# Optimization experiments

Measured on AMD Instinct MI355X. Metric: run time of the kernel, lower is better.

## Reference

```python
import jax, jax.numpy as jnp
import numpy as np

TIMESTEPS = 8
NUM_HEADS = 16
CTX = 1024
D = 1024
HD = D // NUM_HEADS
LN_EPS = 1e-5


def setup_inputs() -> dict:
    key = jax.random.key(0)
    ks = jax.random.split(key, 16)
    s = 0.02
    return {
        "current_embs": jax.random.normal(ks[0], (4, CTX, D), jnp.float32),
        "emb_table": jax.random.normal(ks[1], (TIMESTEPS, D), jnp.float32) * s,
        "Wq": jax.random.normal(ks[2], (NUM_HEADS, D, HD), jnp.float32) * s,
        "Wk": jax.random.normal(ks[3], (NUM_HEADS, D, HD), jnp.float32) * s,
        "Wv": jax.random.normal(ks[4], (NUM_HEADS, D, HD), jnp.float32) * s,
        "fc_w": jax.random.normal(ks[5], (D, D), jnp.float32) * s,
        "fc_b": jnp.zeros((D,), jnp.float32),
        "ln1_w": jnp.ones((D,), jnp.float32),
        "ln1_b": jnp.zeros((D,), jnp.float32),
        "ln2_w": jnp.ones((D,), jnp.float32),
        "ln2_b": jnp.zeros((D,), jnp.float32),
        "mlp_w1": jax.random.normal(ks[6], (D, 2 * D), jnp.float32) * s,
        "mlp_b1": jnp.zeros((2 * D,), jnp.float32),
        "mlp_w2": jax.random.normal(ks[7], (2 * D, D), jnp.float32) * s,
        "mlp_b2": jnp.zeros((D,), jnp.float32),
        "mlp_w3": jax.random.normal(ks[8], (D, D), jnp.float32) * s,
        "mlp_b3": jnp.zeros((D,), jnp.float32),
    }


def _layernorm(x, w, b):
    mu = jnp.mean(x, axis=-1, keepdims=True)
    var = jnp.var(x, axis=-1, keepdims=True)
    return (x - mu) * jax.lax.rsqrt(var + LN_EPS) * w + b


def _block(x, Wq, Wk, Wv, fc_w, fc_b, ln1_w, ln1_b, ln2_w, ln2_b,
           mlp_w1, mlp_b1, mlp_w2, mlp_b2, mlp_w3, mlp_b3):
    B, T, C = x.shape
    h = _layernorm(x, ln1_w, ln1_b)
    # per-head projections: [B,H,T,HD]
    q = jnp.einsum("btd,hdk->bhtk", h, Wq)
    k = jnp.einsum("btd,hdk->bhtk", h, Wk)
    v = jnp.einsum("btd,hdk->bhtk", h, Wv)
    # NOTE: original scales by embed_size**-0.5 (C), not head_dim**-0.5
    wei = jnp.einsum("bhtk,bhsk->bhts", q, k) * (C ** -0.5)
    causal = jnp.tril(jnp.ones((T, T), bool))
    wei = jnp.where(causal, wei, -jnp.inf)
    wei = jax.nn.softmax(wei, axis=-1)
    attn = jnp.einsum("bhts,bhsk->bhtk", wei, v)  # [B,H,T,HD]
    attn = attn.transpose(0, 2, 1, 3).reshape(B, T, C)  # concat heads
    sa = attn @ fc_w + fc_b
    x = x + sa  # dropout is identity in eval mode
    h2 = _layernorm(x, ln2_w, ln2_b)
    m = ((h2 @ mlp_w1 + mlp_b1) @ mlp_w2 + mlp_b2) @ mlp_w3 + mlp_b3
    m = jax.nn.gelu(m, approximate=False)  # GELU after three stacked Linears, as in source
    return x + m


def reference(current_embs, emb_table, Wq, Wk, Wv, fc_w, fc_b,
              ln1_w, ln1_b, ln2_w, ln2_b,
              mlp_w1, mlp_b1, mlp_w2, mlp_b2, mlp_w3, mlp_b3):
    new_embs = current_embs
    for i in range(TIMESTEPS):
        current_embs = current_embs + new_embs + emb_table[i][None, None, :]
        new_embs = _block(current_embs, Wq, Wk, Wv, fc_w, fc_b,
                          ln1_w, ln1_b, ln2_w, ln2_b,
                          mlp_w1, mlp_b1, mlp_w2, mlp_b2, mlp_w3, mlp_b3)
    return new_embs
```

## Files before the change

kernel.cpp:

```cpp
#include <hip/hip_runtime.h>
#include <hip/hip_bf16.h>
#include <math.h>

typedef __bf16 bf16;
typedef __bf16 bf16x8 __attribute__((ext_vector_type(8)));
typedef __bf16 bf16x4 __attribute__((ext_vector_type(4)));
typedef short  s16x4  __attribute__((ext_vector_type(4)));
typedef float  f32x4  __attribute__((ext_vector_type(4)));

#define MFMA32(a,b,c) __builtin_amdgcn_mfma_f32_16x16x32_bf16((a),(b),(c),0,0,0)
#define MFMA16(a,b,c) __builtin_amdgcn_mfma_f32_16x16x16bf16_1k((a),(b),(c),0,0,0)
#define EXP2F(x) __builtin_amdgcn_exp2f(x)
#define GLL16(gp, lp) __builtin_amdgcn_global_load_lds(\
    (const __attribute__((address_space(1))) void*)(gp), \
    (__attribute__((address_space(3))) void*)(lp), 16, 0, 0)

__device__ __forceinline__ float wave_sum(float v){
#pragma unroll
  for(int off=1; off<64; off<<=1) v += __shfl_xor(v, off);
  return v;
}

__global__ __launch_bounds__(256) void add_ln_kernel(
    const float* __restrict__ xsrc, const float* __restrict__ addsrc,
    const float* __restrict__ emb,
    const float* __restrict__ gw, const float* __restrict__ gb,
    float* __restrict__ xout, bf16* __restrict__ hout)
{
  const int row = blockIdx.x;
  const int t = threadIdx.x;
  const size_t rbase = (size_t)row * 1024;
  float4 x = ((const float4*)(xsrc + rbase))[t];
  if(addsrc){
    float4 a = ((const float4*)(addsrc + rbase))[t];
    x.x += a.x; x.y += a.y; x.z += a.z; x.w += a.w;
  }
  if(emb){
    float4 e = ((const float4*)emb)[t];
    x.x += e.x; x.y += e.y; x.z += e.z; x.w += e.w;
  }
  if(xout) ((float4*)(xout + rbase))[t] = x;

  float s = x.x + x.y + x.z + x.w;
  float q = x.x*x.x + x.y*x.y + x.z*x.z + x.w*x.w;
  s = wave_sum(s); q = wave_sum(q);
  __shared__ float red[8];
  const int w = t >> 6;
  if((t & 63) == 0){ red[w] = s; red[4+w] = q; }
  __syncthreads();
  s = red[0]+red[1]+red[2]+red[3];
  q = red[4]+red[5]+red[6]+red[7];
  const float mean = s * (1.0f/1024.0f);
  const float var  = q * (1.0f/1024.0f) - mean*mean;
  const float inv  = rsqrtf(var + 1e-5f);

  float4 wv = ((const float4*)gw)[t];
  float4 bv = ((const float4*)gb)[t];
  bf16x4 hv;
  hv[0] = (bf16)((x.x - mean)*inv*wv.x + bv.x);
  hv[1] = (bf16)((x.y - mean)*inv*wv.y + bv.y);
  hv[2] = (bf16)((x.z - mean)*inv*wv.z + bv.z);
  hv[3] = (bf16)((x.w - mean)*inv*wv.w + bv.w);
  *(bf16x4*)(hout + rbase + t*4) = hv;
}

__global__ __launch_bounds__(256) void pack_qkv3_kernel(
    const float* __restrict__ Wq, const float* __restrict__ Wk, const float* __restrict__ Wv,
    bf16* __restrict__ Wt)
{
  const int i = blockIdx.x*256 + threadIdx.x;
  const int seg = i >> 20, j = i & 1048575;
  const float* W = (seg==0) ? Wq : (seg==1 ? Wk : Wv);
  const int n = j >> 10, d = j & 1023;
  const int h = n >> 6, kk = n & 63;
  Wt[i] = (bf16)W[h*65536 + d*64 + kk];
}
__global__ __launch_bounds__(256) void pack_t_kernel(const float* __restrict__ W, bf16* __restrict__ Wt, int Kd, int Nd){
  const int i = blockIdx.x*256 + threadIdx.x;
  const int n = i / Kd, k = i - n*Kd;
  Wt[i] = (bf16)W[(size_t)k*Nd + n];
}
__global__ __launch_bounds__(256) void pack_cast_kernel(const float* __restrict__ W, bf16* __restrict__ Wb){
  const int i = blockIdx.x*256 + threadIdx.x;
  Wb[i] = (bf16)W[i];
}
__global__ __launch_bounds__(256) void biasmv_kernel(const float* __restrict__ bin, const bf16* __restrict__ WT,
                                                     const float* __restrict__ badd, float* __restrict__ out, int Kd){
  const int n = blockIdx.x, t = threadIdx.x;
  float acc = 0.f;
  for(int k=t; k<Kd; k+=256) acc += bin[k]*(float)WT[(size_t)n*Kd + k];
  acc = wave_sum(acc);
  __shared__ float red[4];
  if((t&63)==0) red[t>>6] = acc;
  __syncthreads();
  if(t==0) out[n] = red[0]+red[1]+red[2]+red[3] + badd[n];
}

template<int EPI, int BLKM>
__global__ __launch_bounds__(256,2) void gemm_kernel(
    const bf16* __restrict__ A, const bf16* __restrict__ Bt,
    float* __restrict__ outf, bf16* __restrict__ outb,
    bf16* __restrict__ o2, bf16* __restrict__ o3,
    const float* __restrict__ bias, const float* __restrict__ res,
    const float* __restrict__ res2, const float* __restrict__ embn,
    int N, int K)
{
  constexpr int RM = BLKM/32;
  constexpr int HM = BLKM/2;
  constexpr int AISS = BLKM/32;
  __shared__ __align__(16) bf16 As[BLKM*64];
  __shared__ __align__(16) bf16 Bs[128*64];
  const int tid = threadIdx.x, w = tid>>6, lane = tid&63;
  const int quad = lane>>4, l16 = lane&15;
  const int wm = w&1, wn = w>>1;
  const int tn = blockIdx.x, tm = blockIdx.y;

  const int srow = lane>>3;
  const int sch  = (lane&7) ^ srow;
  const bf16* Ag = A  + (size_t)(tm*BLKM + w*8 + srow)*K + sch*8;
  const bf16* Bg = Bt + (size_t)(tn*128  + w*8 + srow)*K + sch*8;

  f32x4 acc[RM][4] = {};

  for(int k0 = 0; k0 < K; k0 += 64){
#pragma unroll
    for(int i=0;i<AISS;i++) GLL16(Ag + (size_t)(i*32)*K, As + (w*8 + i*32)*64);
#pragma unroll
    for(int i=0;i<4;i++)    GLL16(Bg + (size_t)(i*32)*K, Bs + (w*8 + i*32)*64);
    Ag += 64; Bg += 64;
    __syncthreads();
    bf16x8 af[RM][2], bfr[4][2];
#pragma unroll
    for(int r=0;r<RM;r++){
      const int row = wm*HM + r*16 + l16;
      const bf16* rp = As + row*64;
#pragma unroll
      for(int kc=0;kc<2;kc++)
        af[r][kc] = *(const bf16x8*)(rp + ((kc*4+quad) ^ (row&7))*8);
    }
#pragma unroll
    for(int c=0;c<4;c++){
      const int row = wn*64 + c*16 + l16;
      const bf16* rp = Bs + row*64;
#pragma unroll
      for(int kc=0;kc<2;kc++)
        bfr[c][kc] = *(const bf16x8*)(rp + ((kc*4+quad) ^ (row&7))*8);
    }
#pragma unroll
    for(int kc=0;kc<2;kc++)
#pragma unroll
      for(int r=0;r<RM;r++)
#pragma unroll
        for(int c=0;c<4;c++)
          acc[r][c] = MFMA32(af[r][kc], bfr[c][kc], acc[r][c]);
    __syncthreads();
  }

#pragma unroll
  for(int r=0;r<RM;r++){
    const int grow0 = tm*BLKM + wm*HM + r*16 + quad*4;
#pragma unroll
    for(int c=0;c<4;c++){
      const int gcol = tn*128 + wn*64 + c*16 + l16;
      float bv = 0.0f;
      if constexpr (EPI>=1 && EPI!=4) bv = bias[gcol];
      if constexpr (EPI==4){
        const int seg = gcol >> 10;
        if(seg < 2){
          bf16* op = (seg==0) ? outb : o2;
          const float qs = (seg==0) ? 0.045084439f : 1.0f;
          const int col = gcol & 1023;
#pragma unroll
          for(int g=0; g<4; g++)
            op[(size_t)(grow0+g)*1024 + col] = (bf16)(acc[r][c][g]*qs);
        } else {
          const int col0 = gcol & 1023, hh = col0>>6, kk = col0&63;
          const int btok = grow0>>10, t0 = grow0&1023;
          bf16x4 pv;
#pragma unroll
          for(int g=0; g<4; g++) pv[g] = (bf16)acc[r][c][g];
          *(bf16x4*)(o3 + ((size_t)(btok*16+hh)*64 + kk)*1024 + t0) = pv;
        }
      } else {
        const float ev = (EPI==5) ? embn[gcol] : 0.0f;
#pragma unroll
        for(int g=0; g<4; g++){
          const float vv = acc[r][c][g] + bv;
          const size_t idx = (size_t)(grow0+g)*N + gcol;
          if constexpr (EPI<=1){
            outb[idx] = (bf16)vv;
          } else if constexpr (EPI==2){
            outf[idx] = res[idx] + vv;
          } else if constexpr (EPI==3){
            const float gel = 0.5f*vv*(1.0f + erff(vv*0.70710678118654752f));
            outf[idx] = res[idx] + gel;
          } else {
            const float gel = 0.5f*vv*(1.0f + erff(vv*0.70710678118654752f));
            outf[idx] = res[idx] + gel + res2[idx] + ev;
          }
        }
      }
    }
  }
}

constexpr int KSZ = 64*64;

__global__ __launch_bounds__(256,4) void attn_kernel(
    const bf16* __restrict__ Q, const bf16* __restrict__ Km,
    const bf16* __restrict__ Vt, bf16* __restrict__ O)
{
  __shared__ __align__(16) bf16 Ks[2*KSZ];
  __shared__ __align__(16) bf16 Vs[2*KSZ];
  const int qt = blockIdx.y;
  const int bh = blockIdx.x;
  const int b = bh >> 4, h = bh & 15;
  const int tid = threadIdx.x;
  const int w = tid>>6, lane = tid&63, quad = lane>>4, l16 = lane&15;
  const size_t qbase = (size_t)b*1024*1024 + (size_t)h*64;
  const size_t vbase = (size_t)(bh*64)*1024;
  const int qrow0 = qt*64 + w*16;
  const int myrow = qrow0 + l16;

  const bf16* qp = Q + qbase + (size_t)myrow*1024 + quad*8;
  bf16x8 bq0 = *(const bf16x8*)qp, bq1 = *(const bf16x8*)(qp + 32);

  f32x4 o[4] = {};
  float l = 0.f;
  const f32x4 zf = {0.f,0.f,0.f,0.f};

  const int srow = lane>>3;
  const int sch  = (lane&7) ^ srow;
  const bf16* kg = Km + qbase + (size_t)(w*8 + srow)*1024 + sch*8;
  const bf16* vg = Vt + vbase + (size_t)(w*8 + srow)*1024 + sch*8;

  GLL16(kg,                       Ks + w*512);
  GLL16(kg + (size_t)32*1024,     Ks + 2048 + w*512);
  GLL16(vg,                       Vs + w*512);
  GLL16(vg + (size_t)32*1024,     Vs + 2048 + w*512);

  for(int kb = 0; kb <= qt; kb++){
    const int cur = kb & 1;
    __syncthreads();

    if(kb < qt){
      const bf16* kgp = kg + (size_t)(kb+1)*64*1024;
      const bf16* vgp = vg + (size_t)(kb+1)*64;
      bf16* kd = Ks + (cur^1)*KSZ + w*512;
      bf16* vd = Vs + (cur^1)*KSZ + w*512;
      GLL16(kgp,                   kd);
      GLL16(kgp + (size_t)32*1024, kd + 2048);
      GLL16(vgp,                   vd);
      GLL16(vgp + (size_t)32*1024, vd + 2048);
    }

    const bool diag = (kb == qt);
    const int nc = diag ? (w+1) : 4;
    const bf16* ksb = Ks + cur*KSZ;
    const bf16* vsb = Vs + cur*KSZ;

    f32x4 s[4];
#pragma unroll
    for(int c=0;c<4;c++){
      if(c >= nc) continue;
      const int row = c*16 + l16;
      const bf16* rp = ksb + row*64;
      bf16x8 ak0 = *(const bf16x8*)(rp + (( quad      ^ (row&7))<<3));
      bf16x8 ak1 = *(const bf16x8*)(rp + (((quad^4)   ^ (row&7))<<3));
      s[c] = MFMA32(ak0, bq0, zf);
      s[c] = MFMA32(ak1, bq1, s[c]);
    }

    s16x4 pp[4];
#pragma unroll
    for(int c=0;c<4;c++){
      if(c >= nc) continue;
      bf16x4 pb;
#pragma unroll
      for(int g=0;g<4;g++){
        const int key = kb*64 + c*16 + quad*4 + g;
        const float e = (diag && key > myrow) ? 0.f : EXP2F(s[c][g]);
        l += e; pb[g] = (bf16)e;
      }
      pp[c] = __builtin_bit_cast(s16x4, pb);
    }

#pragma unroll
    for(int c=0;c<4;c++){
      if(c >= nc) continue;
#pragma unroll
      for(int d=0;d<4;d++){
        const int row = d*16 + l16;
        const int eo  = ((((c*2 + (quad>>1)) ^ (row&7))<<3) + ((quad&1)<<2));
        bf16x4 av = *(const bf16x4*)(vsb + row*64 + eo);
        o[d] = MFMA16(__builtin_bit_cast(s16x4, av), pp[c], o[d]);
      }
    }
  }

  l += __shfl_xor(l, 16); l += __shfl_xor(l, 32);

  __syncthreads();
  {
    bf16* ot = Ks + w*(16*72);
    const float inv = 1.0f / l;
#pragma unroll
    for(int d=0;d<4;d++)
#pragma unroll
      for(int g=0;g<4;g++)
        ot[l16*72 + d*16 + quad*4 + g] = (bf16)(o[d][g]*inv);
#pragma unroll
    for(int p2=0;p2<2;p2++){
      const int qr = (lane>>3) + 8*p2, hd0 = (lane&7)*8;
      bf16x8 val = *(const bf16x8*)(ot + qr*72 + hd0);
      *(bf16x8*)(O + qbase + (size_t)(qrow0+qr)*1024 + hd0) = val;
    }
  }
}

extern "C" void kernel_launch(void* const* d_in, const int* in_sizes, int n_in,
                              void* d_out, int out_size, void* d_ws, size_t ws_size,
                              hipStream_t stream)
{
  const float* x_in = (const float*)d_in[0];
  const float* emb  = (const float*)d_in[1];
  const float* Wq   = (const float*)d_in[2];
  const float* Wk   = (const float*)d_in[3];
  const float* Wv   = (const float*)d_in[4];
  const float* fcw  = (const float*)d_in[5];
  const float* fcb  = (const float*)d_in[6];
  const float* ln1w = (const float*)d_in[7];
  const float* ln1b = (const float*)d_in[8];
  const float* ln2w = (const float*)d_in[9];
  const float* ln2b = (const float*)d_in[10];
  const float* w1   = (const float*)d_in[11];
  const float* b1   = (const float*)d_in[12];
  const float* w2   = (const float*)d_in[13];
  const float* b2   = (const float*)d_in[14];
  const float* w3   = (const float*)d_in[15];
  const float* b3   = (const float*)d_in[16];

  char* ws = (char*)d_ws;
  const size_t MB = 1024*1024;
  float* cur    = (float*)(ws + 0);
  float* x1     = (float*)(ws + 16*MB);
  bf16*  hb     = (bf16*)(ws + 48*MB);
  bf16*  attnb  = (bf16*)(ws + 56*MB);
  bf16*  qb     = (bf16*)(ws + 64*MB);
  bf16*  kbuf   = (bf16*)(ws + 72*MB);
  bf16*  vtb    = (bf16*)(ws + 80*MB);
  bf16*  w1pl   = (bf16*)(ws + 88*MB);
  bf16*  T12    = (bf16*)(ws + 92*MB);
  bf16*  wqkvT  = (bf16*)(ws + 96*MB);
  bf16*  fcT    = (bf16*)(ws + 102*MB);
  bf16*  w2T    = (bf16*)(ws + 104*MB);
  bf16*  w3T    = (bf16*)(ws + 108*MB);
  bf16*  WeffT  = (bf16*)(ws + 110*MB);
  float* tmpb   = (float*)(ws + 112*MB);
  float* beff   = (float*)(ws + 112*MB + 8192);

  pack_qkv3_kernel<<<12288,256,0,stream>>>(Wq, Wk, Wv, wqkvT);
  pack_t_kernel<<<4096,256,0,stream>>>(fcw, fcT, 1024, 1024);
  pack_t_kernel<<<8192,256,0,stream>>>(w2,  w2T, 2048, 1024);
  pack_t_kernel<<<4096,256,0,stream>>>(w3,  w3T, 1024, 1024);
  pack_cast_kernel<<<8192,256,0,stream>>>(w1, w1pl);
  gemm_kernel<0,64><<<dim3(8,16),256,0,stream>>>(w1pl, w2T, nullptr, T12,   nullptr, nullptr, nullptr, nullptr, nullptr, nullptr, 1024, 2048);
  gemm_kernel<0,64><<<dim3(8,16),256,0,stream>>>(w3T,  T12, nullptr, WeffT, nullptr, nullptr, nullptr, nullptr, nullptr, nullptr, 1024, 1024);
  biasmv_kernel<<<1024,256,0,stream>>>(b1,   w2T, b2, tmpb, 2048);
  biasmv_kernel<<<1024,256,0,stream>>>(tmpb, w3T, b3, beff, 1024);

  add_ln_kernel<<<4096,256,0,stream>>>(x_in, x_in, emb, ln1w, ln1b, cur, hb);
  for(int t=0; t<8; t++){
    if(t > 0)
      add_ln_kernel<<<4096,256,0,stream>>>(cur, nullptr, nullptr, ln1w, ln1b, nullptr, hb);
    gemm_kernel<4,128><<<dim3(24,32),256,0,stream>>>(hb, wqkvT, nullptr, qb, kbuf, vtb, nullptr, nullptr, nullptr, nullptr, 3072, 1024);
    attn_kernel<<<dim3(64,16),256,0,stream>>>(qb, kbuf, vtb, attnb);
    gemm_kernel<2,64><<<dim3(8,64),256,0,stream>>>(attnb, fcT, x1, nullptr, nullptr, nullptr, fcb, cur, nullptr, nullptr, 1024, 1024);
    add_ln_kernel<<<4096,256,0,stream>>>(x1, nullptr, nullptr, ln2w, ln2b, nullptr, hb);
    if(t < 7)
      gemm_kernel<5,64><<<dim3(8,64),256,0,stream>>>(hb, WeffT, cur, nullptr, nullptr, nullptr, beff, x1, cur, emb + (t+1)*1024, 1024, 1024);
    else
      gemm_kernel<3,64><<<dim3(8,64),256,0,stream>>>(hb, WeffT, (float*)d_out, nullptr, nullptr, nullptr, beff, x1, nullptr, nullptr, 1024, 1024);
  }
}
```

Baseline: 1.130 ms.

## Load attention K/V tiles directly from global memory instead of LDS staging

The attention kernel no longer double-buffers K and V tiles into shared memory with async global-to-LDS loads and block barriers. Each wave now reads its MFMA operands straight from global memory, relying on L1/L2 caching, and the per-block barriers are gone. The output staging uses a small dedicated buffer with vectorized bf16x4 stores, and the occupancy hint in the launch bounds is dropped. This removes synchronization and LDS traffic but adds redundant, less coalesced global loads across the four waves and exposes global latency without a prefetch.

After: 1.736 ms. +53.6%, slower.

```diff
diff --git a/kernel.cpp b/kernel.cpp
--- a/kernel.cpp
+++ b/kernel.cpp
@@ -204,14 +204,11 @@
   }
 }
 
-constexpr int KSZ = 64*64;
-
-__global__ __launch_bounds__(256,4) void attn_kernel(
+__global__ __launch_bounds__(256) void attn_kernel(
     const bf16* __restrict__ Q, const bf16* __restrict__ Km,
     const bf16* __restrict__ Vt, bf16* __restrict__ O)
 {
-  __shared__ __align__(16) bf16 Ks[2*KSZ];
-  __shared__ __align__(16) bf16 Vs[2*KSZ];
+  __shared__ __align__(16) bf16 obuf[4][16*72];
   const int qt = blockIdx.y;
   const int bh = blockIdx.x;
   const int b = bh >> 4, h = bh & 15;
@@ -225,48 +222,26 @@
   const bf16* qp = Q + qbase + (size_t)myrow*1024 + quad*8;
   bf16x8 bq0 = *(const bf16x8*)qp, bq1 = *(const bf16x8*)(qp + 32);
 
+  const bf16* kp = Km + qbase + (size_t)l16*1024 + quad*8;
+  const bf16* vp = Vt + vbase + (size_t)l16*1024 + quad*4;
+
   f32x4 o[4] = {};
   float l = 0.f;
   const f32x4 zf = {0.f,0.f,0.f,0.f};
 
-  const int srow = lane>>3;
-  const int sch  = (lane&7) ^ srow;
-  const bf16* kg = Km + qbase + (size_t)(w*8 + srow)*1024 + sch*8;
-  const bf16* vg = Vt + vbase + (size_t)(w*8 + srow)*1024 + sch*8;
-
-  GLL16(kg,                       Ks + w*512);
-  GLL16(kg + (size_t)32*1024,     Ks + 2048 + w*512);
-  GLL16(vg,                       Vs + w*512);
-  GLL16(vg + (size_t)32*1024,     Vs + 2048 + w*512);
-
   for(int kb = 0; kb <= qt; kb++){
-    const int cur = kb & 1;
-    __syncthreads();
-
-    if(kb < qt){
-      const bf16* kgp = kg + (size_t)(kb+1)*64*1024;
-      const bf16* vgp = vg + (size_t)(kb+1)*64;
-      bf16* kd = Ks + (cur^1)*KSZ + w*512;
-      bf16* vd = Vs + (cur^1)*KSZ + w*512;
-      GLL16(kgp,                   kd);
-      GLL16(kgp + (size_t)32*1024, kd + 2048);
-      GLL16(vgp,                   vd);
-      GLL16(vgp + (size_t)32*1024, vd + 2048);
-    }
-
     const bool diag = (kb == qt);
     const int nc = diag ? (w+1) : 4;
-    const bf16* ksb = Ks + cur*KSZ;
-    const bf16* vsb = Vs + cur*KSZ;
+    const bf16* kpb = kp + (size_t)kb*64*1024;
+    const bf16* vpb = vp + kb*64;
 
     f32x4 s[4];
 #pragma unroll
     for(int c=0;c<4;c++){
       if(c >= nc) continue;
-      const int row = c*16 + l16;
-      const bf16* rp = ksb + row*64;
-      bf16x8 ak0 = *(const bf16x8*)(rp + (( quad      ^ (row&7))<<3));
-      bf16x8 ak1 = *(const bf16x8*)(rp + (((quad^4)   ^ (row&7))<<3));
+      const bf16* rp = kpb + (size_t)(c*16)*1024;
+      bf16x8 ak0 = *(const bf16x8*)rp;
+      bf16x8 ak1 = *(const bf16x8*)(rp + 32);
       s[c] = MFMA32(ak0, bq0, zf);
       s[c] = MFMA32(ak1, bq1, s[c]);
     }
@@ -290,9 +265,7 @@
       if(c >= nc) continue;
 #pragma unroll
       for(int d=0;d<4;d++){
-        const int row = d*16 + l16;
-        const int eo  = ((((c*2 + (quad>>1)) ^ (row&7))<<3) + ((quad&1)<<2));
-        bf16x4 av = *(const bf16x4*)(vsb + row*64 + eo);
+        bf16x4 av = *(const bf16x4*)(vpb + (size_t)(d*16)*1024 + c*16);
         o[d] = MFMA16(__builtin_bit_cast(s16x4, av), pp[c], o[d]);
       }
     }
@@ -300,15 +273,16 @@
 
   l += __shfl_xor(l, 16); l += __shfl_xor(l, 32);
 
-  __syncthreads();
   {
-    bf16* ot = Ks + w*(16*72);
+    bf16* ot = obuf[w];
     const float inv = 1.0f / l;
 #pragma unroll
-    for(int d=0;d<4;d++)
-#pragma unroll
-      for(int g=0;g<4;g++)
-        ot[l16*72 + d*16 + quad*4 + g] = (bf16)(o[d][g]*inv);
+    for(int d=0;d<4;d++){
+      bf16x4 ob;
+#pragma unroll
+      for(int g=0;g<4;g++) ob[g] = (bf16)(o[d][g]*inv);
+      *(bf16x4*)(ot + l16*72 + d*16 + quad*4) = ob;
+    }
 #pragma unroll
     for(int p2=0;p2<2;p2++){
       const int qr = (lane>>3) + 8*p2, hd0 = (lane&7)*8;
```

## Fuse layernorm into GEMM prologue with row stats from producer epilogues

Applied to the files above, without the earlier changes.

Removes the per-step layernorm kernels. Producing GEMM epilogues now accumulate per-row sum and sum-of-squares with atomics into a stats buffer, and a new gemm_ln_kernel normalizes fp32 activations on the fly while staging the A tile to LDS. This drops the bf16 intermediate buffer writes and reads and two launches per timestep. In exchange, the A tile is re-read in fp32 by every column block, global atomics are added, and the A load loses async pipelining. The variance is computed as E[x^2]-mean^2.

New measurement: 1.443 ms. 27.7% more time.

```diff
diff --git a/kernel.cpp b/kernel.cpp
--- a/kernel.cpp
+++ b/kernel.cpp
@@ -21,25 +21,18 @@
   return v;
 }
 
-__global__ __launch_bounds__(256) void add_ln_kernel(
-    const float* __restrict__ xsrc, const float* __restrict__ addsrc,
-    const float* __restrict__ emb,
-    const float* __restrict__ gw, const float* __restrict__ gb,
-    float* __restrict__ xout, bf16* __restrict__ hout)
+__global__ __launch_bounds__(256) void add_stats_kernel(
+    const float* __restrict__ xsrc, const float* __restrict__ emb,
+    float* __restrict__ xout, float* __restrict__ ostats)
 {
   const int row = blockIdx.x;
   const int t = threadIdx.x;
   const size_t rbase = (size_t)row * 1024;
   float4 x = ((const float4*)(xsrc + rbase))[t];
-  if(addsrc){
-    float4 a = ((const float4*)(addsrc + rbase))[t];
-    x.x += a.x; x.y += a.y; x.z += a.z; x.w += a.w;
-  }
-  if(emb){
-    float4 e = ((const float4*)emb)[t];
-    x.x += e.x; x.y += e.y; x.z += e.z; x.w += e.w;
-  }
-  if(xout) ((float4*)(xout + rbase))[t] = x;
+  float4 e = ((const float4*)emb)[t];
+  x.x = 2.0f*x.x + e.x; x.y = 2.0f*x.y + e.y;
+  x.z = 2.0f*x.z + e.z; x.w = 2.0f*x.w + e.w;
+  ((float4*)(xout + rbase))[t] = x;
 
   float s = x.x + x.y + x.z + x.w;
   float q = x.x*x.x + x.y*x.y + x.z*x.z + x.w*x.w;
@@ -48,20 +41,14 @@
   const int w = t >> 6;
   if((t & 63) == 0){ red[w] = s; red[4+w] = q; }
   __syncthreads();
-  s = red[0]+red[1]+red[2]+red[3];
-  q = red[4]+red[5]+red[6]+red[7];
-  const float mean = s * (1.0f/1024.0f);
-  const float var  = q * (1.0f/1024.0f) - mean*mean;
-  const float inv  = rsqrtf(var + 1e-5f);
-
-  float4 wv = ((const float4*)gw)[t];
-  float4 bv = ((const float4*)gb)[t];
-  bf16x4 hv;
-  hv[0] = (bf16)((x.x - mean)*inv*wv.x + bv.x);
-  hv[1] = (bf16)((x.y - mean)*inv*wv.y + bv.y);
-  hv[2] = (bf16)((x.z - mean)*inv*wv.z + bv.z);
-  hv[3] = (bf16)((x.w - mean)*inv*wv.w + bv.w);
-  *(bf16x4*)(hout + rbase + t*4) = hv;
+  if(t == 0){
+    ostats[row]        = red[0]+red[1]+red[2]+red[3];
+    ostats[4096 + row] = red[4]+red[5]+red[6]+red[7];
+  }
+}
+
+__global__ __launch_bounds__(256) void zero_kernel(float* __restrict__ p){
+  ((float4*)p)[blockIdx.x*256 + threadIdx.x] = float4{0.f,0.f,0.f,0.f};
 }
 
 __global__ __launch_bounds__(256) void pack_qkv3_kernel(
@@ -100,10 +87,8 @@
 __global__ __launch_bounds__(256,2) void gemm_kernel(
     const bf16* __restrict__ A, const bf16* __restrict__ Bt,
     float* __restrict__ outf, bf16* __restrict__ outb,
-    bf16* __restrict__ o2, bf16* __restrict__ o3,
     const float* __restrict__ bias, const float* __restrict__ res,
-    const float* __restrict__ res2, const float* __restrict__ embn,
-    int N, int K)
+    float* __restrict__ ostats, int N, int K)
 {
   constexpr int RM = BLKM/32;
   constexpr int HM = BLKM/2;
@@ -156,6 +141,7 @@
     __syncthreads();
   }
 
+  float rs[RM][4] = {}, rq[RM][4] = {};
 #pragma unroll
   for(int r=0;r<RM;r++){
     const int grow0 = tm*BLKM + wm*HM + r*16 + quad*4;
@@ -163,7 +149,150 @@
     for(int c=0;c<4;c++){
       const int gcol = tn*128 + wn*64 + c*16 + l16;
       float bv = 0.0f;
-      if constexpr (EPI>=1 && EPI!=4) bv = bias[gcol];
+      if constexpr (EPI>=1) bv = bias[gcol];
+#pragma unroll
+      for(int g=0; g<4; g++){
+        const float vv = acc[r][c][g] + bv;
+        const size_t idx = (size_t)(grow0+g)*N + gcol;
+        if constexpr (EPI<=1){
+          outb[idx] = (bf16)vv;
+        } else {
+          const float ov = res[idx] + vv;
+          outf[idx] = ov;
+          rs[r][g] += ov; rq[r][g] += ov*ov;
+        }
+      }
+    }
+  }
+  if constexpr (EPI==2){
+#pragma unroll
+    for(int r=0;r<RM;r++)
+#pragma unroll
+      for(int g=0;g<4;g++){
+        float s1 = rs[r][g], s2 = rq[r][g];
+        s1 += __shfl_xor(s1,1); s2 += __shfl_xor(s2,1);
+        s1 += __shfl_xor(s1,2); s2 += __shfl_xor(s2,2);
+        s1 += __shfl_xor(s1,4); s2 += __shfl_xor(s2,4);
+        s1 += __shfl_xor(s1,8); s2 += __shfl_xor(s2,8);
+        if(l16 == 0){
+          const int row = tm*BLKM + wm*HM + r*16 + quad*4 + g;
+          atomicAdd(ostats + row, s1);
+          atomicAdd(ostats + 4096 + row, s2);
+        }
+      }
+  }
+}
+
+template<int EPI, int BLKM>
+__global__ __launch_bounds__(256,2) void gemm_ln_kernel(
+    const float* __restrict__ X, const float* __restrict__ stats,
+    const float* __restrict__ gw, const float* __restrict__ gb,
+    const bf16* __restrict__ Bt,
+    float* __restrict__ outf, bf16* __restrict__ outb,
+    bf16* __restrict__ o2, bf16* __restrict__ o3,
+    const float* __restrict__ bias, const float* __restrict__ res,
+    const float* __restrict__ res2, const float* __restrict__ embn,
+    float* __restrict__ ostats, int N)
+{
+  constexpr int RM  = BLKM/32;
+  constexpr int HM  = BLKM/2;
+  constexpr int RPT = BLKM/32;
+  __shared__ __align__(16) bf16 As[BLKM*64];
+  __shared__ __align__(16) bf16 Bs[128*64];
+  const int tid = threadIdx.x, w = tid>>6, lane = tid&63;
+  const int quad = lane>>4, l16 = lane&15;
+  const int wm = w&1, wn = w>>1;
+  const int tn = blockIdx.x, tm = blockIdx.y;
+
+  const int srow = lane>>3;
+  const int sch  = (lane&7) ^ srow;
+  const bf16* Bg = Bt + (size_t)(tn*128 + w*8 + srow)*1024 + sch*8;
+
+  const int c8  = tid & 7;
+  const int rr0 = (tid>>3)*RPT;
+  float mean_[RPT], inv_[RPT];
+#pragma unroll
+  for(int i=0;i<RPT;i++){
+    const int row = tm*BLKM + rr0 + i;
+    const float mu = stats[row]*(1.0f/1024.0f);
+    mean_[i] = mu;
+    inv_[i]  = rsqrtf(stats[4096+row]*(1.0f/1024.0f) - mu*mu + 1e-5f);
+  }
+  const float* xp = X + (size_t)(tm*BLKM + rr0)*1024 + c8*8;
+
+  float4 xa[RPT][2];
+#pragma unroll
+  for(int i=0;i<RPT;i++){
+    xa[i][0] = *(const float4*)(xp + (size_t)i*1024);
+    xa[i][1] = *(const float4*)(xp + (size_t)i*1024 + 4);
+  }
+  float4 gv0 = *(const float4*)(gw + c8*8), gv1 = *(const float4*)(gw + c8*8 + 4);
+  float4 bv0 = *(const float4*)(gb + c8*8), bv1 = *(const float4*)(gb + c8*8 + 4);
+
+  f32x4 acc[RM][4] = {};
+
+  for(int k0 = 0; k0 < 1024; k0 += 64){
+    __syncthreads();
+#pragma unroll
+    for(int i=0;i<RPT;i++){
+      bf16x8 hv;
+      hv[0] = (bf16)((xa[i][0].x - mean_[i])*inv_[i]*gv0.x + bv0.x);
+      hv[1] = (bf16)((xa[i][0].y - mean_[i])*inv_[i]*gv0.y + bv0.y);
+      hv[2] = (bf16)((xa[i][0].z - mean_[i])*inv_[i]*gv0.z + bv0.z);
+      hv[3] = (bf16)((xa[i][0].w - mean_[i])*inv_[i]*gv0.w + bv0.w);
+      hv[4] = (bf16)((xa[i][1].x - mean_[i])*inv_[i]*gv1.x + bv1.x);
+      hv[5] = (bf16)((xa[i][1].y - mean_[i])*inv_[i]*gv1.y + bv1.y);
+      hv[6] = (bf16)((xa[i][1].z - mean_[i])*inv_[i]*gv1.z + bv1.z);
+      hv[7] = (bf16)((xa[i][1].w - mean_[i])*inv_[i]*gv1.w + bv1.w);
+      *(bf16x8*)(As + (rr0+i)*64 + ((c8 ^ ((rr0+i)&7))<<3)) = hv;
+    }
+#pragma unroll
+    for(int i=0;i<4;i++) GLL16(Bg + (size_t)(i*32)*1024, Bs + (w*8 + i*32)*64);
+    Bg += 64;
+    __syncthreads();
+    if(k0 + 64 < 1024){
+      const float* xn = xp + k0 + 64;
+#pragma unroll
+      for(int i=0;i<RPT;i++){
+        xa[i][0] = *(const float4*)(xn + (size_t)i*1024);
+        xa[i][1] = *(const float4*)(xn + (size_t)i*1024 + 4);
+      }
+      gv0 = *(const float4*)(gw + k0+64 + c8*8); gv1 = *(const float4*)(gw + k0+64 + c8*8 + 4);
+      bv0 = *(const float4*)(gb + k0+64 + c8*8); bv1 = *(const float4*)(gb + k0+64 + c8*8 + 4);
+    }
+    bf16x8 af[RM][2], bfr[4][2];
+#pragma unroll
+    for(int r=0;r<RM;r++){
+      const int row = wm*HM + r*16 + l16;
+      const bf16* rp = As + row*64;
+#pragma unroll
+      for(int kc=0;kc<2;kc++)
+        af[r][kc] = *(const bf16x8*)(rp + ((kc*4+quad) ^ (row&7))*8);
+    }
+#pragma unroll
+    for(int c=0;c<4;c++){
+      const int row = wn*64 + c*16 + l16;
+      const bf16* rp = Bs + row*64;
+#pragma unroll
+      for(int kc=0;kc<2;kc++)
+        bfr[c][kc] = *(const bf16x8*)(rp + ((kc*4+quad) ^ (row&7))*8);
+    }
+#pragma unroll
+    for(int kc=0;kc<2;kc++)
+#pragma unroll
+      for(int r=0;r<RM;r++)
+#pragma unroll
+        for(int c=0;c<4;c++)
+          acc[r][c] = MFMA32(af[r][kc], bfr[c][kc], acc[r][c]);
+  }
+
+  float rs[RM][4] = {}, rq[RM][4] = {};
+#pragma unroll
+  for(int r=0;r<RM;r++){
+    const int grow0 = tm*BLKM + wm*HM + r*16 + quad*4;
+#pragma unroll
+    for(int c=0;c<4;c++){
+      const int gcol = tn*128 + wn*64 + c*16 + l16;
       if constexpr (EPI==4){
         const int seg = gcol >> 10;
         if(seg < 2){
@@ -182,25 +311,40 @@
           *(bf16x4*)(o3 + ((size_t)(btok*16+hh)*64 + kk)*1024 + t0) = pv;
         }
       } else {
+        const float bv = bias[gcol];
         const float ev = (EPI==5) ? embn[gcol] : 0.0f;
 #pragma unroll
         for(int g=0; g<4; g++){
           const float vv = acc[r][c][g] + bv;
           const size_t idx = (size_t)(grow0+g)*N + gcol;
-          if constexpr (EPI<=1){
-            outb[idx] = (bf16)vv;
-          } else if constexpr (EPI==2){
-            outf[idx] = res[idx] + vv;
-          } else if constexpr (EPI==3){
-            const float gel = 0.5f*vv*(1.0f + erff(vv*0.70710678118654752f));
+          const float gel = 0.5f*vv*(1.0f + erff(vv*0.70710678118654752f));
+          if constexpr (EPI==3){
             outf[idx] = res[idx] + gel;
           } else {
-            const float gel = 0.5f*vv*(1.0f + erff(vv*0.70710678118654752f));
-            outf[idx] = res[idx] + gel + res2[idx] + ev;
+            const float ov = res[idx] + gel + res2[idx] + ev;
+            outf[idx] = ov;
+            rs[r][g] += ov; rq[r][g] += ov*ov;
           }
         }
       }
     }
+  }
+  if constexpr (EPI==5){
+#pragma unroll
+    for(int r=0;r<RM;r++)
+#pragma unroll
+      for(int g=0;g<4;g++){
+        float s1 = rs[r][g], s2 = rq[r][g];
+        s1 += __shfl_xor(s1,1); s2 += __shfl_xor(s2,1);
+        s1 += __shfl_xor(s1,2); s2 += __shfl_xor(s2,2);
+        s1 += __shfl_xor(s1,4); s2 += __shfl_xor(s2,4);
+        s1 += __shfl_xor(s1,8); s2 += __shfl_xor(s2,8);
+        if(l16 == 0){
+          const int row = tm*BLKM + wm*HM + r*16 + quad*4 + g;
+          atomicAdd(ostats + row, s1);
+          atomicAdd(ostats + 4096 + row, s2);
+        }
+      }
   }
 }
 
@@ -229,10 +373,11 @@
   float l = 0.f;
   const f32x4 zf = {0.f,0.f,0.f,0.f};
 
-  const int srow = lane>>3;
-  const int sch  = (lane&7) ^ srow;
-  const bf16* kg = Km + qbase + (size_t)(w*8 + srow)*1024 + sch*8;
-  const bf16* vg = Vt + vbase + (size_t)(w*8 + srow)*1024 + sch*8;
+  const int srow2 = tid>>3;
+  const int sc = (tid&7) ^ (srow2&7);
+  const bf16* kg = Km + qbase + (size_t)(w*8 + (lane>>3))*1024 + ((lane&7)^(lane>>3))*8;
+  const bf16* vg = Vt + vbase + (size_t)(w*8 + (lane>>3))*1024 + ((lane&7)^(lane>>3))*8;
+  (void)srow2; (void)sc;
 
   GLL16(kg,                       Ks + w*512);
   GLL16(kg + (size_t)32*1024,     Ks + 2048 + w*512);
@@ -344,7 +489,6 @@
   const size_t MB = 1024*1024;
   float* cur    = (float*)(ws + 0);
   float* x1     = (float*)(ws + 16*MB);
-  bf16*  hb     = (bf16*)(ws + 48*MB);
   bf16*  attnb  = (bf16*)(ws + 56*MB);
   bf16*  qb     = (bf16*)(ws + 64*MB);
   bf16*  kbuf   = (bf16*)(ws + 72*MB);
@@ -358,28 +502,33 @@
   bf16*  WeffT  = (bf16*)(ws + 110*MB);
   float* tmpb   = (float*)(ws + 112*MB);
   float* beff   = (float*)(ws + 112*MB + 8192);
-
+  float* statsb = (float*)(ws + 113*MB);
+
+  zero_kernel<<<128,256,0,stream>>>(statsb);
   pack_qkv3_kernel<<<12288,256,0,stream>>>(Wq, Wk, Wv, wqkvT);
   pack_t_kernel<<<4096,256,0,stream>>>(fcw, fcT, 1024, 1024);
   pack_t_kernel<<<8192,256,0,stream>>>(w2,  w2T, 2048, 1024);
   pack_t_kernel<<<4096,256,0,stream>>>(w3,  w3T, 1024, 1024);
   pack_cast_kernel<<<8192,256,0,stream>>>(w1, w1pl);
-  gemm_kernel<0,64><<<dim3(8,16),256,0,stream>>>(w1pl, w2T, nullptr, T12,   nullptr, nullptr, nullptr, nullptr, nullptr, nullptr, 1024, 2048);
-  gemm_kernel<0,64><<<dim3(8,16),256,0,stream>>>(w3T,  T12, nullptr, WeffT, nullptr, nullptr, nullptr, nullptr, nullptr, nullptr, 1024, 1024);
+  gemm_kernel<0,64><<<dim3(8,16),256,0,stream>>>(w1pl, w2T, nullptr, T12,   nullptr, nullptr, nullptr, 1024, 2048);
+  gemm_kernel<0,64><<<dim3(8,16),256,0,stream>>>(w3T,  T12, nullptr, WeffT, nullptr, nullptr, nullptr, 1024, 1024);
   biasmv_kernel<<<1024,256,0,stream>>>(b1,   w2T, b2, tmpb, 2048);
   biasmv_kernel<<<1024,256,0,stream>>>(tmpb, w3T, b3, beff, 1024);
 
-  add_ln_kernel<<<4096,256,0,stream>>>(x_in, x_in, emb, ln1w, ln1b, cur, hb);
+  add_stats_kernel<<<4096,256,0,stream>>>(x_in, emb, cur, statsb);
   for(int t=0; t<8; t++){
-    if(t > 0)
-      add_ln_kernel<<<4096,256,0,stream>>>(cur, nullptr, nullptr, ln1w, ln1b, nullptr, hb);
-    gemm_kernel<4,128><<<dim3(24,32),256,0,stream>>>(hb, wqkvT, nullptr, qb, kbuf, vtb, nullptr, nullptr, nullptr, nullptr, 3072, 1024);
+    float* s1 = statsb + (size_t)(2*t  )*8192;
+    float* s2 = statsb + (size_t)(2*t+1)*8192;
+    float* s1n = statsb + (size_t)(2*t+2)*8192;
+    gemm_ln_kernel<4,128><<<dim3(24,32),256,0,stream>>>(cur, s1, ln1w, ln1b, wqkvT,
+        nullptr, qb, kbuf, vtb, nullptr, nullptr, nullptr, nullptr, nullptr, 3072);
     attn_kernel<<<dim3(64,16),256,0,stream>>>(qb, kbuf, vtb, attnb);
-    gemm_kernel<2,64><<<dim3(8,64),256,0,stream>>>(attnb, fcT, x1, nullptr, nullptr, nullptr, fcb, cur, nullptr, nullptr, 1024, 1024);
-    add_ln_kernel<<<4096,256,0,stream>>>(x1, nullptr, nullptr, ln2w, ln2b, nullptr, hb);
+    gemm_kernel<2,64><<<dim3(8,64),256,0,stream>>>(attnb, fcT, x1, nullptr, fcb, cur, s2, 1024, 1024);
     if(t < 7)
-      gemm_kernel<5,64><<<dim3(8,64),256,0,stream>>>(hb, WeffT, cur, nullptr, nullptr, nullptr, beff, x1, cur, emb + (t+1)*1024, 1024, 1024);
+      gemm_ln_kernel<5,64><<<dim3(8,64),256,0,stream>>>(x1, s2, ln2w, ln2b, WeffT,
+          cur, nullptr, nullptr, nullptr, beff, x1, cur, emb + (t+1)*1024, s1n, 1024);
     else
-      gemm_kernel<3,64><<<dim3(8,64),256,0,stream>>>(hb, WeffT, (float*)d_out, nullptr, nullptr, nullptr, beff, x1, nullptr, nullptr, 1024, 1024);
-  }
-}
+      gemm_ln_kernel<3,64><<<dim3(8,64),256,0,stream>>>(x1, s2, ln2w, ln2b, WeffT,
+          (float*)d_out, nullptr, nullptr, nullptr, beff, x1, nullptr, nullptr, nullptr, 1024);
+  }
+}
```
